# Optimization experiments

Hardware: AMD Instinct MI355X
Metric: run time of the kernel (lower is better)

Reference implementation:

```python
import jax, jax.numpy as jnp
import numpy as np

B, CIN, CMID, COUT, H, W = 4, 64, 128, 128, 128, 128
K = 9  # 3x3 taps
EPS = 1e-5


def conv3x3(x, w, b):
    # standard 3x3 conv, stride 1, pad 1, NCHW / OIHW
    y = jax.lax.conv_general_dilated(x, w, (1, 1), ((1, 1), (1, 1)),
                                     dimension_numbers=('NCHW', 'OIHW', 'NCHW'))
    return y + b[None, :, None, None]


def deform_conv3x3(x, offset, w, b):
    # torchvision DeformConv2d semantics (v1, no mask), kernel 3, pad 1, stride 1.
    # offset: [B, 2*K, H, W] with per-tap (dy, dx) pairs.
    Bn, C, Hn, Wn = x.shape
    off = offset.reshape(Bn, K, 2, Hn, Wn)
    off_y, off_x = off[:, :, 0], off[:, :, 1]          # [B,K,H,W]
    ky = (jnp.arange(K) // 3).astype(x.dtype)          # tap row 0..2
    kx = (jnp.arange(K) % 3).astype(x.dtype)           # tap col 0..2
    # sampling positions: p = out_pos - pad + tap + offset
    py = jnp.arange(Hn, dtype=x.dtype)[None, None, :, None] - 1.0 + ky[None, :, None, None] + off_y
    px = jnp.arange(Wn, dtype=x.dtype)[None, None, None, :] - 1.0 + kx[None, :, None, None] + off_x
    y0 = jnp.floor(py); x0 = jnp.floor(px)
    wy1 = py - y0; wx1 = px - x0                       # bilinear fractions
    y0i = y0.astype(jnp.int32); x0i = x0.astype(jnp.int32)
    xf = x.reshape(Bn, C, Hn * Wn)

    def gather(iy, ix):
        valid = ((iy >= 0) & (iy < Hn) & (ix >= 0) & (ix < Wn)).astype(x.dtype)
        idx = jnp.clip(iy, 0, Hn - 1) * Wn + jnp.clip(ix, 0, Wn - 1)  # [B,K,H,W]
        g = jax.vmap(lambda xb, ib: xb[:, ib])(xf, idx)               # [B,C,K,H,W]
        return g, valid

    g00, v00 = gather(y0i, x0i)
    g01, v01 = gather(y0i, x0i + 1)
    g10, v10 = gather(y0i + 1, x0i)
    g11, v11 = gather(y0i + 1, x0i + 1)

    def wmul(g, v, wgt):
        return g * (v * wgt)[:, None]                  # broadcast over channel dim

    sampled = (wmul(g00, v00, (1 - wy1) * (1 - wx1)) +
               wmul(g01, v01, (1 - wy1) * wx1) +
               wmul(g10, v10, wy1 * (1 - wx1)) +
               wmul(g11, v11, wy1 * wx1))              # [B,C,K,H,W]
    out = jnp.einsum('bckhw,ock->bohw', sampled, w.reshape(w.shape[0], C, K))
    return out + b[None, :, None, None]


def batchnorm_relu(x, gamma, beta):
    # training-mode BN: batch statistics over (N,H,W), biased variance
    mean = jnp.mean(x, axis=(0, 2, 3), keepdims=True)
    var = jnp.mean(jnp.square(x - mean), axis=(0, 2, 3), keepdims=True)
    y = (x - mean) * jax.lax.rsqrt(var + EPS)
    return jax.nn.relu(y * gamma[None, :, None, None] + beta[None, :, None, None])


def setup_inputs() -> dict:
    key = jax.random.key(0)
    ks = jax.random.split(key, 13)
    s = 0.05  # small weights keep offsets small / sampling mostly in-bounds
    return {
        'x': jax.random.normal(ks[0], (B, CIN, H, W), jnp.float32),
        'w_off1': jax.random.normal(ks[1], (2 * K, CIN, 3, 3), jnp.float32) * s,
        'b_off1': jnp.zeros((2 * K,), jnp.float32),
        'w1': jax.random.normal(ks[2], (CMID, CIN, 3, 3), jnp.float32) * s,
        'b1': jax.random.normal(ks[3], (CMID,), jnp.float32) * s,
        'g1': jnp.ones((CMID,), jnp.float32),
        'be1': jnp.zeros((CMID,), jnp.float32),
        'w_off2': jax.random.normal(ks[4], (2 * K, CMID, 3, 3), jnp.float32) * s,
        'b_off2': jnp.zeros((2 * K,), jnp.float32),
        'w2': jax.random.normal(ks[5], (COUT, CMID, 3, 3), jnp.float32) * s,
        'b2': jax.random.normal(ks[6], (COUT,), jnp.float32) * s,
        'g2': jnp.ones((COUT,), jnp.float32),
        'be2': jnp.zeros((COUT,), jnp.float32),
    }


def reference(x, w_off1, b_off1, w1, b1, g1, be1, w_off2, b_off2, w2, b2, g2, be2):
    offset1 = conv3x3(x, w_off1, b_off1)
    out = deform_conv3x3(x, offset1, w1, b1)
    out = batchnorm_relu(out, g1, be1)
    offset2 = conv3x3(out, w_off2, b_off2)
    out = deform_conv3x3(out, offset2, w2, b2)
    out = batchnorm_relu(out, g2, be2)
    return out
```

## Files before the change

kernel.cpp:

```cpp
#include <hip/hip_runtime.h>
#include <hip/hip_bf16.h>

#define BB 4
#define H_ 128
#define W_ 128
#define HWP 16384
#define CIN1 64
#define CMID 128
#define KOFF 18

typedef short short8 __attribute__((ext_vector_type(8)));
typedef float floatx4 __attribute__((ext_vector_type(4)));

#define WS_AB   16
#define WS_CVT  288
#define CVT_TOTAL 4447396
#define WS_WF1  4447744
#define WS_WF2  4484608
#define WS_XT   4558336
#define WS_OFF  6655488
#define WS_Y1   7835136
#define WS_Y1T  16223744
#define WS_WFO1 20418048
#define WS_WFO2 20436480
#define WS_PART 21600000
#define WS_Y2   WS_Y1

#define R_X     0
#define R_WOFF1 4194304
#define R_BOFF1 4204672
#define R_W1    4204690
#define R_B1    4278418
#define R_G1    4278546
#define R_BE1   4278674
#define R_WOFF2 4278802
#define R_BOFF2 4299538
#define R_W2    4299556
#define R_B2    4447012
#define R_G2    4447140
#define R_BE2   4447268

struct SrcPtrs { const void* p[13]; };

__device__ inline short f2bf(float f) {
    __hip_bfloat16 h = __float2bfloat16(f);
    return *reinterpret_cast<short*>(&h);
}
__device__ inline float bf2f(unsigned short u) {
    return __uint_as_float(((unsigned int)u) << 16);
}
__device__ inline float bfu_lo(unsigned int u) { return __uint_as_float(u << 16); }
__device__ inline float bfu_hi(unsigned int u) { return __uint_as_float(u & 0xFFFF0000u); }
__device__ inline float rl_f(float v, int i) {
    return __int_as_float(__builtin_amdgcn_readlane(__float_as_int(v), i));
}

__global__ void probe_dtype_k(const unsigned int* __restrict__ g1, int* __restrict__ flag) {
    if (threadIdx.x == 0 && blockIdx.x == 0) {
        flag[0] = ((g1[0] & 0xFFFFu) != 0u) ? 1 : 0;
    }
}

__global__ __launch_bounds__(256) void convert_inputs_k(SrcPtrs sp, float* __restrict__ dst,
                                                        const int* __restrict__ flag, int total) {
    int i = blockIdx.x * 256 + threadIdx.x;
    if (i >= total) return;
    constexpr int prefix[13] = {0, R_WOFF1, R_BOFF1, R_W1, R_B1, R_G1, R_BE1,
                                R_WOFF2, R_BOFF2, R_W2, R_B2, R_G2, R_BE2};
    const void* src = sp.p[0];
    int base = 0;
#pragma unroll
    for (int q = 1; q < 13; ++q) {
        if (i >= prefix[q]) { src = sp.p[q]; base = prefix[q]; }
    }
    int local = i - base;
    float v;
    if (flag[0] != 0) {
        v = bf2f(((const unsigned short*)src)[local]);
    } else {
        v = ((const float*)src)[local];
    }
    dst[i] = v;
}

template <int CIN>
__global__ __launch_bounds__(256) void wf_build_k(const float* __restrict__ w, short* __restrict__ wf) {
    constexpr int KSTEPS = CIN * 9 / 32;
    int idx = blockIdx.x * 256 + threadIdx.x;
    int j    = idx & 7;
    int lane = (idx >> 3) & 63;
    int rem  = idx >> 9;
    int ks   = rem % KSTEPS;
    int ct   = rem / KSTEPS;
    int co = ct * 16 + (lane & 15);
    int k  = ks * 32 + (lane >> 4) * 8 + j;
    int ci = k & (CIN - 1);
    int kk = k / CIN;
    wf[idx] = f2bf(w[(co * CIN + ci) * 9 + kk]);
}

template <int CIN>
__global__ __launch_bounds__(256) void wf_off_build_k(const float* __restrict__ w, short* __restrict__ wf) {
    constexpr int KSTEPS = CIN * 9 / 32;
    int idx = blockIdx.x * 256 + threadIdx.x;
    int j    = idx & 7;
    int lane = (idx >> 3) & 63;
    int rem  = idx >> 9;
    int ks   = rem % KSTEPS;
    int cc   = rem / KSTEPS;
    int sel  = cc >> 1;
    int co = (cc & 1) * 16 + (lane & 15);
    int k  = ks * 32 + (lane >> 4) * 8 + j;
    int ci = k & (CIN - 1);
    int kk = k / CIN;
    float v = (co < KOFF) ? w[(co * CIN + ci) * 9 + kk] : 0.f;
    short hi = f2bf(v);
    wf[idx] = sel ? f2bf(v - bf2f((unsigned short)hi)) : hi;
}

__global__ __launch_bounds__(256) void xt_build_k(const float* __restrict__ x,
                                                  unsigned short* __restrict__ xt,
                                                  unsigned short* __restrict__ xtl) {
    __shared__ __align__(4) short s_t[64 * 66];
    __shared__ __align__(4) short s_tl[64 * 66];
    int bi  = blockIdx.x;
    int hw0 = (bi & 255) * 64;
    int b   = bi >> 8;
    int t   = threadIdx.x;
    int hwp = t & 63;
#pragma unroll
    for (int it = 0; it < 16; ++it) {
        int c = it * 4 + (t >> 6);
        float v = x[((long)(b * 64 + c) << 14) + hw0 + hwp];
        short hi = f2bf(v);
        s_t[hwp * 66 + c]  = hi;
        s_tl[hwp * 66 + c] = f2bf(v - bf2f((unsigned short)hi));
    }
    __syncthreads();
#pragma unroll
    for (int it = 0; it < 8; ++it) {
        int i  = it * 256 + t;
        int c2 = (i & 31) * 2;
        int hw2 = i >> 5;
        long da = ((long)((b << 14) + hw0 + hw2)) * 64 + c2;
        *(int*)&xt[da]  = *(const int*)&s_t[hw2 * 66 + c2];
        *(int*)&xtl[da] = *(const int*)&s_tl[hw2 * 66 + c2];
    }
}

__device__ inline int conv_tpk(int h, int w0, int lane, int wv) {
    int tpk = 0;
    if (lane < 36) {
        int r = wv + 8 * lane;
        int p = r & 31;
        int k = r >> 5;
        int y = h - 1 + k / 3;
        int x = w0 + p - 1 + (k % 3);
        int valid = (y >= 0 && y < H_ && x >= 0 && x < W_) ? 1 : 0;
        int yc = min(max(y, 0), H_ - 1), xc = min(max(x, 0), W_ - 1);
        tpk = (yc * W_ + xc) | (valid << 16);
    }
    return tpk;
}

__device__ inline void convgather64(const unsigned short* __restrict__ xb, short* __restrict__ s_samp,
                                    int half, int li, int wv, int tpk) {
    constexpr int PADc = 584;
    unsigned int ub[18];
#pragma unroll
    for (int j = 0; j < 18; ++j) {
        int pkA = __builtin_amdgcn_readlane(tpk, 2 * j);
        int pkB = __builtin_amdgcn_readlane(tpk, 2 * j + 1);
        int pk = half ? pkB : pkA;
        unsigned int u = *(const unsigned int*)(xb + (pk & 0xFFFF) * 64 + 2 * li);
        ub[j] = (pk >> 16) ? u : 0u;
    }
#pragma unroll
    for (int j = 0; j < 18; ++j) {
        int r = wv + 8 * (half ? (2 * j + 1) : (2 * j));
        *(unsigned int*)&s_samp[(r & 31) * PADc + (r >> 5) * 64 + 2 * li] = ub[j];
    }
}

template <int I0, int NJ, int KKB>
__device__ inline void convgather128(const unsigned short* __restrict__ xb, short* __restrict__ s_samp,
                                     int lane, int wv, int tpk) {
    constexpr int PADc = 648;
    unsigned int ub[NJ];
#pragma unroll
    for (int j = 0; j < NJ; ++j) {
        int pk = __builtin_amdgcn_readlane(tpk, I0 + j);
        unsigned int u = *(const unsigned int*)(xb + (pk & 0xFFFF) * 128 + 2 * lane);
        ub[j] = (pk >> 16) ? u : 0u;
    }
#pragma unroll
    for (int j = 0; j < NJ; ++j) {
        int r = wv + 8 * (I0 + j);
        *(unsigned int*)&s_samp[(r & 31) * PADc + ((r >> 5) - KKB) * 128 + 2 * lane] = ub[j];
    }
}

__global__ __launch_bounds__(512, 4) void conv_off_mfma64_k(const unsigned short* __restrict__ xt,
                                                            const unsigned short* __restrict__ xtl,
                                                            const short* __restrict__ wfo,
                                                            const float* __restrict__ bias,
                                                            float* __restrict__ off) {
    constexpr int KSTEPS = 18;
    constexpr int PADc = 584;
    __shared__ __align__(16) short s_samp[32 * PADc];
    __shared__ float s_red[4 * 256];

    int bi = blockIdx.x;
    int w0 = (bi & 3) * 32;
    int h  = (bi >> 2) & 127;
    int b  = bi >> 9;
    int t  = threadIdx.x;
    int lane = t & 63;
    int wv   = t >> 6;

    int tpk = conv_tpk(h, w0, lane, wv);
    const unsigned short* xbh = xt  + (long)b * HWP * 64;
    const unsigned short* xbl = xtl + (long)b * HWP * 64;
    int half = lane >> 5, li = lane & 31;

    int p_   = lane & 15;
    int quad = lane >> 4;
    int c   = wv & 3;
    int ksl = wv >> 2;
    int ct  = c & 1;
    int pt  = c >> 1;
    int row = pt * 16 + p_;
    floatx4 acc;
#pragma unroll
    for (int r = 0; r < 4; ++r) {
        int co = ct * 16 + quad * 4 + r;
        acc[r] = (ksl == 0 && co < KOFF) ? bias[co] : 0.f;
    }

    convgather64(xbh, s_samp, half, li, wv, tpk);
    __syncthreads();
#pragma unroll
    for (int ki = 0; ki < 9; ++ki) {
        int ks = ksl * 9 + ki;
        short8 bfr = *(const short8*)&s_samp[row * PADc + ks * 32 + quad * 8];
        short8 ah  = *(const short8*)&wfo[(((long)ct * KSTEPS + ks) * 64 + lane) * 8];
        short8 al  = *(const short8*)&wfo[(((long)(2 + ct) * KSTEPS + ks) * 64 + lane) * 8];
        acc = __builtin_amdgcn_mfma_f32_16x16x32_bf16(ah, bfr, acc, 0, 0, 0);
        acc = __builtin_amdgcn_mfma_f32_16x16x32_bf16(al, bfr, acc, 0, 0, 0);
    }
    __syncthreads();

    convgather64(xbl, s_samp, half, li, wv, tpk);
    __syncthreads();
#pragma unroll
    for (int ki = 0; ki < 9; ++ki) {
        int ks = ksl * 9 + ki;
        short8 bfr = *(const short8*)&s_samp[row * PADc + ks * 32 + quad * 8];
        short8 ah  = *(const short8*)&wfo[(((long)ct * KSTEPS + ks) * 64 + lane) * 8];
        acc = __builtin_amdgcn_mfma_f32_16x16x32_bf16(ah, bfr, acc, 0, 0, 0);
    }

    if (ksl == 1) {
#pragma unroll
        for (int r = 0; r < 4; ++r) s_red[c * 256 + (quad * 4 + r) * 16 + p_] = acc[r];
    }
    __syncthreads();
    if (ksl == 0) {
#pragma unroll
        for (int r = 0; r < 4; ++r) {
            int co = ct * 16 + quad * 4 + r;
            if (co < KOFF) {
                float v = acc[r] + s_red[c * 256 + (quad * 4 + r) * 16 + p_];
                off[((long)(b * KOFF + co) << 14) + (h << 7) + w0 + pt * 16 + p_] = v;
            }
        }
    }
}

__global__ __launch_bounds__(512, 4) void conv_off_mfma128_k(const unsigned short* __restrict__ xt,
                                                             const unsigned short* __restrict__ xtl,
                                                             const short* __restrict__ wfo,
                                                             const float* __restrict__ bias,
                                                             float* __restrict__ off) {
    constexpr int KSTEPS = 36;
    constexpr int PADc = 648;
    __shared__ __align__(16) short s_samp[32 * PADc];
    __shared__ float s_red[4 * 256];

    int bi = blockIdx.x;
    int w0 = (bi & 3) * 32;
    int h  = (bi >> 2) & 127;
    int b  = bi >> 9;
    int t  = threadIdx.x;
    int lane = t & 63;
    int wv   = t >> 6;

    int tpk = conv_tpk(h, w0, lane, wv);
    const unsigned short* xbh = xt  + (long)b * HWP * 128;
    const unsigned short* xbl = xtl + (long)b * HWP * 128;

    int p_   = lane & 15;
    int quad = lane >> 4;
    int c   = wv & 3;
    int ksl = wv >> 2;
    int ct  = c & 1;
    int pt  = c >> 1;
    int row = pt * 16 + p_;
    floatx4 acc;
#pragma unroll
    for (int r = 0; r < 4; ++r) {
        int co = ct * 16 + quad * 4 + r;
        acc[r] = (ksl == 0 && co < KOFF) ? bias[co] : 0.f;
    }

    convgather128<0, 16, 0>(xbh, s_samp, lane, wv, tpk);
    __syncthreads();
#pragma unroll
    for (int ki = 0; ki < 8; ++ki) {
        int ks = ksl * 8 + ki;
        short8 bfr = *(const short8*)&s_samp[row * PADc + ks * 32 + quad * 8];
        short8 ah  = *(const short8*)&wfo[(((long)ct * KSTEPS + ks) * 64 + lane) * 8];
        short8 al  = *(const short8*)&wfo[(((long)(2 + ct) * KSTEPS + ks) * 64 + lane) * 8];
        acc = __builtin_amdgcn_mfma_f32_16x16x32_bf16(ah, bfr, acc, 0, 0, 0);
        acc = __builtin_amdgcn_mfma_f32_16x16x32_bf16(al, bfr, acc, 0, 0, 0);
    }
    __syncthreads();

    convgather128<16, 20, 4>(xbh, s_samp, lane, wv, tpk);
    __syncthreads();
#pragma unroll
    for (int ki = 0; ki < 10; ++ki) {
        int ks = 16 + ksl * 10 + ki;
        short8 bfr = *(const short8*)&s_samp[row * PADc + (ks - 16) * 32 + quad * 8];
        short8 ah  = *(const short8*)&wfo[(((long)ct * KSTEPS + ks) * 64 + lane) * 8];
        short8 al  = *(const short8*)&wfo[(((long)(2 + ct) * KSTEPS + ks) * 64 + lane) * 8];
        acc = __builtin_amdgcn_mfma_f32_16x16x32_bf16(ah, bfr, acc, 0, 0, 0);
        acc = __builtin_amdgcn_mfma_f32_16x16x32_bf16(al, bfr, acc, 0, 0, 0);
    }
    __syncthreads();

    convgather128<0, 16, 0>(xbl, s_samp, lane, wv, tpk);
    __syncthreads();
#pragma unroll
    for (int ki = 0; ki < 8; ++ki) {
        int ks = ksl * 8 + ki;
        short8 bfr = *(const short8*)&s_samp[row * PADc + ks * 32 + quad * 8];
        short8 ah  = *(const short8*)&wfo[(((long)ct * KSTEPS + ks) * 64 + lane) * 8];
        acc = __builtin_amdgcn_mfma_f32_16x16x32_bf16(ah, bfr, acc, 0, 0, 0);
    }
    __syncthreads();

    convgather128<16, 20, 4>(xbl, s_samp, lane, wv, tpk);
    __syncthreads();
#pragma unroll
    for (int ki = 0; ki < 10; ++ki) {
        int ks = 16 + ksl * 10 + ki;
        short8 bfr = *(const short8*)&s_samp[row * PADc + (ks - 16) * 32 + quad * 8];
        short8 ah  = *(const short8*)&wfo[(((long)ct * KSTEPS + ks) * 64 + lane) * 8];
        acc = __builtin_amdgcn_mfma_f32_16x16x32_bf16(ah, bfr, acc, 0, 0, 0);
    }

    if (ksl == 1) {
#pragma unroll
        for (int r = 0; r < 4; ++r) s_red[c * 256 + (quad * 4 + r) * 16 + p_] = acc[r];
    }
    __syncthreads();
    if (ksl == 0) {
#pragma unroll
        for (int r = 0; r < 4; ++r) {
            int co = ct * 16 + quad * 4 + r;
            if (co < KOFF) {
                float v = acc[r] + s_red[c * 256 + (quad * 4 + r) * 16 + p_];
                off[((long)(b * KOFF + co) << 14) + (h << 7) + w0 + pt * 16 + p_] = v;
            }
        }
    }
}

__device__ inline void build_table2(const float* __restrict__ off,
                                    int b, int h, int w0, int lane, int wv,
                                    int& tpk, float& tw0, float& tw1, float& tw2, float& tw3) {
    tpk = 0; tw0 = tw1 = tw2 = tw3 = 0.f;
    if (lane < 36) {
        int r = wv + 8 * lane;
        int p = r & 31;
        int k = r >> 5;
        int wpix = w0 + p;
        long obase = ((long)(b * KOFF) << 14) + (h << 7) + wpix;
        float oy = off[obase + ((long)(2 * k) << 14)];
        float ox = off[obase + ((long)(2 * k + 1) << 14)];
        float py = (float)(h - 1 + (k / 3)) + oy;
        float px = (float)(wpix - 1 + (k % 3)) + ox;
        float fy = floorf(py), fx = floorf(px);
        float wy = py - fy, wx = px - fx;
        int y0 = (int)fy, x0 = (int)fx;
        int y1 = y0 + 1, x1 = x0 + 1;
        bool vy0 = (y0 >= 0) && (y0 < H_);
        bool vy1 = (y1 >= 0) && (y1 < H_);
        bool vx0 = (x0 >= 0) && (x0 < W_);
        bool vx1 = (x1 >= 0) && (x1 < W_);
        float wy0 = 1.f - wy, wx0 = 1.f - wx;
        tw0 = (vy0 && vx0) ? wy0 * wx0 : 0.f;
        tw1 = (vy0 && vx1) ? wy0 * wx  : 0.f;
        tw2 = (vy1 && vx0) ? wy  * wx0 : 0.f;
        tw3 = (vy1 && vx1) ? wy  * wx  : 0.f;
        int iy0 = min(max(y0, 0), H_ - 1), iy1 = min(max(y1, 0), H_ - 1);
        int ix0 = min(max(x0, 0), W_ - 1), ix1 = min(max(x1, 0), W_ - 1);
        int dx = ix1 - ix0;
        int dy = iy1 - iy0;
        tpk = (iy0 * W_ + ix0) | (dx << 14) | (dy << 15);
    }
}

template <int NB>
__device__ inline void gather_batch128v2(const unsigned short* __restrict__ xb, short* __restrict__ s_samp,
                                         int i0, int kkbase, int wv, int lane,
                                         int tpk, float tw0, float tw1, float tw2, float tw3) {
    constexpr int PADc = 648;
    uint4 ub[NB];
#pragma unroll
    for (int j = 0; j < NB; ++j) {
        int pk = __builtin_amdgcn_readlane(tpk, i0 + j);
        const unsigned short* b00 = xb + (pk & 0x3FFF) * 128;
        const unsigned short* b01 = b00 + ((pk >> 14) & 1) * 128;
        const unsigned short* b10 = b00 + ((pk >> 15) & 1) * (W_ * 128);
        const unsigned short* b11 = b01 + ((pk >> 15) & 1) * (W_ * 128);
        ub[j].x = *(const unsigned int*)(b00 + 2 * lane);
        ub[j].y = *(const unsigned int*)(b01 + 2 * lane);
        ub[j].z = *(const unsigned int*)(b10 + 2 * lane);
        ub[j].w = *(const unsigned int*)(b11 + 2 * lane);
    }
#pragma unroll
    for (int j = 0; j < NB; ++j) {
        int i = i0 + j;
        int r = wv + 8 * i;
        float w00 = rl_f(tw0, i), w01 = rl_f(tw1, i), w10 = rl_f(tw2, i), w11 = rl_f(tw3, i);
        float vlo = w00 * bfu_lo(ub[j].x) + w01 * bfu_lo(ub[j].y)
                  + w10 * bfu_lo(ub[j].z) + w11 * bfu_lo(ub[j].w);
        float vhi = w00 * bfu_hi(ub[j].x) + w01 * bfu_hi(ub[j].y)
                  + w10 * bfu_hi(ub[j].z) + w11 * bfu_hi(ub[j].w);
        __hip_bfloat162 h2 = __float22bfloat162_rn(make_float2(vlo, vhi));
        *(unsigned int*)&s_samp[(r & 31) * PADc + ((r >> 5) - kkbase) * 128 + 2 * lane] =
            *reinterpret_cast<unsigned int*>(&h2);
    }
}

template <int NBP>
__device__ inline void gather_batch64v2(const unsigned short* __restrict__ xb, short* __restrict__ s_samp,
                                        int i0, int wv, int half, int li,
                                        int tpk, float tw0, float tw1, float tw2, float tw3) {
    constexpr int PADc = 584;
    uint4 ub[NBP];
#pragma unroll
    for (int j = 0; j < NBP; ++j) {
        int iA = i0 + 2 * j, iB = iA + 1;
        int pkA = __builtin_amdgcn_readlane(tpk, iA);
        int pkB = __builtin_amdgcn_readlane(tpk, iB);
        int pk = half ? pkB : pkA;
        const unsigned short* b00 = xb + (pk & 0x3FFF) * 64;
        const unsigned short* b01 = b00 + ((pk >> 14) & 1) * 64;
        const unsigned short* b10 = b00 + ((pk >> 15) & 1) * (W_ * 64);
        const unsigned short* b11 = b01 + ((pk >> 15) & 1) * (W_ * 64);
        ub[j].x = *(const unsigned int*)(b00 + 2 * li);
        ub[j].y = *(const unsigned int*)(b01 + 2 * li);
        ub[j].z = *(const unsigned int*)(b10 + 2 * li);
        ub[j].w = *(const unsigned int*)(b11 + 2 * li);
    }
#pragma unroll
    for (int j = 0; j < NBP; ++j) {
        int iA = i0 + 2 * j, iB = iA + 1;
        float w00 = half ? rl_f(tw0, iB) : rl_f(tw0, iA);
        float w01 = half ? rl_f(tw1, iB) : rl_f(tw1, iA);
        float w10 = half ? rl_f(tw2, iB) : rl_f(tw2, iA);
        float w11 = half ? rl_f(tw3, iB) : rl_f(tw3, iA);
        float vlo = w00 * bfu_lo(ub[j].x) + w01 * bfu_lo(ub[j].y)
                  + w10 * bfu_lo(ub[j].z) + w11 * bfu_lo(ub[j].w);
        float vhi = w00 * bfu_hi(ub[j].x) + w01 * bfu_hi(ub[j].y)
                  + w10 * bfu_hi(ub[j].z) + w11 * bfu_hi(ub[j].w);
        __hip_bfloat162 h2 = __float22bfloat162_rn(make_float2(vlo, vhi));
        int r = wv + 8 * (half ? iB : iA);
        *(unsigned int*)&s_samp[(r & 31) * PADc + (r >> 5) * 64 + 2 * li] =
            *reinterpret_cast<unsigned int*>(&h2);
    }
}

__global__ __launch_bounds__(512, 4) void deform_mfma64_k(const unsigned short* __restrict__ xt,
                                                          const float* __restrict__ off,
                                                          const short* __restrict__ wf,
                                                          const float* __restrict__ bias,
                                                          float* __restrict__ out) {
    constexpr int KSTEPS = 18;
    constexpr int PADc = 584;
    __shared__ __align__(16) short s_samp[32 * PADc];

    int bi = blockIdx.x;
    int w0 = (bi & 3) * 32;
    int h  = (bi >> 2) & 127;
    int b  = bi >> 9;
    int t  = threadIdx.x;
    int lane = t & 63;
    int wv   = t >> 6;

    int tpk; float tw0, tw1, tw2, tw3;
    build_table2(off, b, h, w0, lane, wv, tpk, tw0, tw1, tw2, tw3);
    const unsigned short* xb = xt + (long)b * HWP * 64;
    int half = lane >> 5, li = lane & 31;

    gather_batch64v2<6>(xb, s_samp,  0, wv, half, li, tpk, tw0, tw1, tw2, tw3);
    gather_batch64v2<6>(xb, s_samp, 12, wv, half, li, tpk, tw0, tw1, tw2, tw3);
    gather_batch64v2<6>(xb, s_samp, 24, wv, half, li, tpk, tw0, tw1, tw2, tw3);
    __syncthreads();

    int p_   = lane & 15;
    int quad = lane >> 4;
    int ct = wv;
    floatx4 acc0, acc1;
#pragma unroll
    for (int r = 0; r < 4; ++r) {
        float bv = bias[ct * 16 + quad * 4 + r];
        acc0[r] = bv;
        acc1[r] = bv;
    }
#pragma unroll 3
    for (int ks = 0; ks < KSTEPS; ++ks) {
        short8 a  = *(const short8*)&wf[(((long)ct * KSTEPS + ks) * 64 + lane) * 8];
        short8 b0 = *(const short8*)&s_samp[p_ * PADc + ks * 32 + quad * 8];
        short8 b1 = *(const short8*)&s_samp[(16 + p_) * PADc + ks * 32 + quad * 8];
        acc0 = __builtin_amdgcn_mfma_f32_16x16x32_bf16(a, b0, acc0, 0, 0, 0);
        acc1 = __builtin_amdgcn_mfma_f32_16x16x32_bf16(a, b1, acc1, 0, 0, 0);
    }

    long ob = ((long)(b * 128) << 14) + (h << 7) + w0 + p_;
#pragma unroll
    for (int r = 0; r < 4; ++r) {
        long cpl = (long)(ct * 16 + quad * 4 + r) << 14;
        out[ob + cpl]      = acc0[r];
        out[ob + 16 + cpl] = acc1[r];
    }
}

__global__ __launch_bounds__(512, 4) void deform_mfma128_k(const unsigned short* __restrict__ xt,
                                                           const float* __restrict__ off,
                                                           const short* __restrict__ wf,
                                                           const float* __restrict__ bias,
                                                           float* __restrict__ out) {
    constexpr int KSTEPS = 36;
    constexpr int PADc = 648;
    __shared__ __align__(16) short s_samp[32 * PADc];

    int bi = blockIdx.x;
    int w0 = (bi & 3) * 32;
    int h  = (bi >> 2) & 127;
    int b  = bi >> 9;
    int t  = threadIdx.x;
    int lane = t & 63;
    int wv   = t >> 6;

    int tpk; float tw0, tw1, tw2, tw3;
    build_table2(off, b, h, w0, lane, wv, tpk, tw0, tw1, tw2, tw3);
    const unsigned short* xb = xt + (long)b * HWP * 128;

    int p_   = lane & 15;
    int quad = lane >> 4;
    int ct = wv;
    floatx4 acc0, acc1;
#pragma unroll
    for (int r = 0; r < 4; ++r) {
        float bv = bias[ct * 16 + quad * 4 + r];
        acc0[r] = bv;
        acc1[r] = bv;
    }

    gather_batch128v2<8>(xb, s_samp, 0, 0, wv, lane, tpk, tw0, tw1, tw2, tw3);
    gather_batch128v2<8>(xb, s_samp, 8, 0, wv, lane, tpk, tw0, tw1, tw2, tw3);
    __syncthreads();
#pragma unroll 4
    for (int ks = 0; ks < 16; ++ks) {
        short8 a  = *(const short8*)&wf[(((long)ct * KSTEPS + ks) * 64 + lane) * 8];
        short8 b0 = *(const short8*)&s_samp[p_ * PADc + ks * 32 + quad * 8];
        short8 b1 = *(const short8*)&s_samp[(16 + p_) * PADc + ks * 32 + quad * 8];
        acc0 = __builtin_amdgcn_mfma_f32_16x16x32_bf16(a, b0, acc0, 0, 0, 0);
        acc1 = __builtin_amdgcn_mfma_f32_16x16x32_bf16(a, b1, acc1, 0, 0, 0);
    }
    __syncthreads();

    gather_batch128v2<5>(xb, s_samp, 16, 4, wv, lane, tpk, tw0, tw1, tw2, tw3);
    gather_batch128v2<5>(xb, s_samp, 21, 4, wv, lane, tpk, tw0, tw1, tw2, tw3);
    gather_batch128v2<5>(xb, s_samp, 26, 4, wv, lane, tpk, tw0, tw1, tw2, tw3);
    gather_batch128v2<5>(xb, s_samp, 31, 4, wv, lane, tpk, tw0, tw1, tw2, tw3);
    __syncthreads();
#pragma unroll 4
    for (int ks = 16; ks < KSTEPS; ++ks) {
        short8 a  = *(const short8*)&wf[(((long)ct * KSTEPS + ks) * 64 + lane) * 8];
        short8 b0 = *(const short8*)&s_samp[p_ * PADc + (ks - 16) * 32 + quad * 8];
        short8 b1 = *(const short8*)&s_samp[(16 + p_) * PADc + (ks - 16) * 32 + quad * 8];
        acc0 = __builtin_amdgcn_mfma_f32_16x16x32_bf16(a, b0, acc0, 0, 0, 0);
        acc1 = __builtin_amdgcn_mfma_f32_16x16x32_bf16(a, b1, acc1, 0, 0, 0);
    }

    long ob = ((long)(b * 128) << 14) + (h << 7) + w0 + p_;
#pragma unroll
    for (int r = 0; r < 4; ++r) {
        long cpl = (long)(ct * 16 + quad * 4 + r) << 14;
        out[ob + cpl]      = acc0[r];
        out[ob + 16 + cpl] = acc1[r];
    }
}

__global__ __launch_bounds__(256) void bn_stats_part_k(const float* __restrict__ y, float* __restrict__ part) {
    int bi = blockIdx.x;
    int c = bi & 127;
    int b = bi >> 7;
    int t = threadIdx.x;
    const float4* p4 = (const float4*)(y + ((long)(b * 128 + c) << 14));
    float sum = 0.f, ss = 0.f;
#pragma unroll
    for (int i = 0; i < 16; ++i) {
        float4 v = p4[t + 256 * i];
        sum += v.x + v.y + v.z + v.w;
        ss  += v.x * v.x + v.y * v.y + v.z * v.z + v.w * v.w;
    }
#pragma unroll
    for (int o = 32; o > 0; o >>= 1) { sum += __shfl_down(sum, o); ss += __shfl_down(ss, o); }
    __shared__ float s1[4], s2[4];
    int wave = t >> 6;
    if ((t & 63) == 0) { s1[wave] = sum; s2[wave] = ss; }
    __syncthreads();
    if (t == 0) {
        part[bi]       = s1[0] + s1[1] + s1[2] + s1[3];
        part[512 + bi] = s2[0] + s2[1] + s2[2] + s2[3];
    }
}

__global__ __launch_bounds__(256) void bn_apply_dual_k(float* __restrict__ y, const float* __restrict__ part,
                                                       const float* __restrict__ g, const float* __restrict__ be,
                                                       unsigned short* __restrict__ yt,
                                                       unsigned short* __restrict__ ytl) {
    __shared__ __align__(4) short s_t[64 * 134];
    __shared__ __align__(4) short s_tl[64 * 134];
    __shared__ float s_a[128], s_sh[128];
    int t = threadIdx.x;
    if (t < 128) {
        float sum = part[t] + part[128 + t] + part[256 + t] + part[384 + t];
        float ss  = part[512 + t] + part[640 + t] + part[768 + t] + part[896 + t];
        float mean = sum * (1.f / 65536.f);
        float var  = ss  * (1.f / 65536.f) - mean * mean;
        float inv  = rsqrtf(var + 1e-5f);
        float a = g[t] * inv;
        s_a[t]  = a;
        s_sh[t] = be[t] - mean * a;
    }
    __syncthreads();

    int bi  = blockIdx.x;
    int hw0 = (bi & 255) * 64;
    int b   = bi >> 8;
    int hwp = t & 63;
#pragma unroll 4
    for (int it = 0; it < 32; ++it) {
        int c = it * 4 + (t >> 6);
        float a = s_a[c], sh = s_sh[c];
        long addr = ((long)(b * 128 + c) << 14) + hw0 + hwp;
        float v = y[addr];
        v = fmaxf(v * a + sh, 0.f);
        y[addr] = v;
        short hi = f2bf(v);
        s_t[hwp * 134 + c]  = hi;
        s_tl[hwp * 134 + c] = f2bf(v - bf2f((unsigned short)hi));
    }
    __syncthreads();
#pragma unroll 4
    for (int it = 0; it < 16; ++it) {
        int i   = it * 256 + t;
        int c2  = (i & 63) * 2;
        int hw2 = i >> 6;
        long da = ((long)((b << 14) + hw0 + hw2)) * 128 + c2;
        *(int*)&yt[da]  = *(const int*)&s_t[hw2 * 134 + c2];
        *(int*)&ytl[da] = *(const int*)&s_tl[hw2 * 134 + c2];
    }
}

__global__ __launch_bounds__(256) void bn_apply_out_k(const float* __restrict__ y, const float* __restrict__ part,
                                                      const float* __restrict__ g, const float* __restrict__ be,
                                                      const int* __restrict__ flag, void* __restrict__ out, int total4) {
    __shared__ float s_a[128], s_sh[128];
    int t = threadIdx.x;
    if (t < 128) {
        float sum = part[t] + part[128 + t] + part[256 + t] + part[384 + t];
        float ss  = part[512 + t] + part[640 + t] + part[768 + t] + part[896 + t];
        float mean = sum * (1.f / 65536.f);
        float var  = ss  * (1.f / 65536.f) - mean * mean;
        float inv  = rsqrtf(var + 1e-5f);
        float a = g[t] * inv;
        s_a[t]  = a;
        s_sh[t] = be[t] - mean * a;
    }
    __syncthreads();

    int i = blockIdx.x * 256 + t;
    if (i >= total4) return;
    int c = (i >> 12) & 127;
    float a = s_a[c], sh = s_sh[c];
    float4 v = reinterpret_cast<const float4*>(y)[i];
    v.x = fmaxf(v.x * a + sh, 0.f);
    v.y = fmaxf(v.y * a + sh, 0.f);
    v.z = fmaxf(v.z * a + sh, 0.f);
    v.w = fmaxf(v.w * a + sh, 0.f);
    if (flag[0] != 0) {
        ushort4 u;
        u.x = (unsigned short)f2bf(v.x);
        u.y = (unsigned short)f2bf(v.y);
        u.z = (unsigned short)f2bf(v.z);
        u.w = (unsigned short)f2bf(v.w);
        reinterpret_cast<ushort4*>(out)[i] = u;
    } else {
        reinterpret_cast<float4*>(out)[i] = v;
    }
}

extern "C" void kernel_launch(void* const* d_in, const int* in_sizes, int n_in,
                              void* d_out, int out_size, void* d_ws, size_t ws_size,
                              hipStream_t stream) {
    float* ws   = (float*)d_ws;
    int*   flag = (int*)d_ws;
    float* cvt  = ws + WS_CVT;

    const float* X     = cvt + R_X;
    const float* Woff1 = cvt + R_WOFF1;
    const float* Boff1 = cvt + R_BOFF1;
    const float* W1f   = cvt + R_W1;
    const float* B1f   = cvt + R_B1;
    const float* G1    = cvt + R_G1;
    const float* Be1   = cvt + R_BE1;
    const float* Woff2 = cvt + R_WOFF2;
    const float* Boff2 = cvt + R_BOFF2;
    const float* W2f   = cvt + R_W2;
    const float* B2f   = cvt + R_B2;
    const float* G2    = cvt + R_G2;
    const float* Be2   = cvt + R_BE2;

    short* WF1  = (short*)(ws + WS_WF1);
    short* WF2  = (short*)(ws + WS_WF2);
    short* WFO1 = (short*)(ws + WS_WFO1);
    short* WFO2 = (short*)(ws + WS_WFO2);
    unsigned short* XT   = (unsigned short*)(ws + WS_XT);
    unsigned short* XTL  = (unsigned short*)(ws + WS_Y1);
    unsigned short* Y1T  = (unsigned short*)(ws + WS_Y1T);
    unsigned short* Y1TL = (unsigned short*)(ws + WS_CVT);
    float* OFF  = ws + WS_OFF;
    float* PART = ws + WS_PART;
    float* Y1   = ws + WS_Y1;
    float* Y2   = ws + WS_Y2;

    SrcPtrs sp;
    for (int j = 0; j < 13; ++j) sp.p[j] = d_in[j];

    probe_dtype_k<<<1, 64, 0, stream>>>((const unsigned int*)d_in[5], flag);
    convert_inputs_k<<<(CVT_TOTAL + 255) / 256, 256, 0, stream>>>(sp, cvt, flag, CVT_TOTAL);
    wf_build_k<64><<<288, 256, 0, stream>>>(W1f, WF1);
    wf_build_k<128><<<576, 256, 0, stream>>>(W2f, WF2);
    wf_off_build_k<64><<<144, 256, 0, stream>>>(Woff1, WFO1);
    wf_off_build_k<128><<<288, 256, 0, stream>>>(Woff2, WFO2);
    xt_build_k<<<1024, 256, 0, stream>>>(X, XT, XTL);

    conv_off_mfma64_k<<<BB * 128 * 4, 512, 0, stream>>>(XT, XTL, WFO1, Boff1, OFF);
    deform_mfma64_k<<<BB * 128 * 4, 512, 0, stream>>>(XT, OFF, WF1, B1f, Y1);
    bn_stats_part_k<<<512, 256, 0, stream>>>(Y1, PART);
    bn_apply_dual_k<<<1024, 256, 0, stream>>>(Y1, PART, G1, Be1, Y1T, Y1TL);

    conv_off_mfma128_k<<<BB * 128 * 4, 512, 0, stream>>>(Y1T, Y1TL, WFO2, Boff2, OFF);
    deform_mfma128_k<<<BB * 128 * 4, 512, 0, stream>>>(Y1T, OFF, WF2, B2f, Y2);
    bn_stats_part_k<<<512, 256, 0, stream>>>(Y2, PART);
    bn_apply_out_k<<<(BB * 128 * HWP / 4 + 255) / 256, 256, 0, stream>>>(Y2, PART, G2, Be2, flag, d_out, BB * 128 * HWP / 4);
}
```

Before: 343.2 us.

## Fuse offset conv into deformable conv kernels, keeping offsets in LDS

Merges the offset-predicting 3x3 conv kernel into the deformable conv kernel for both layers. Each block computes its 18 offset channels for the same 32-pixel tile, writes them to shared memory, and builds the bilinear sampling table from there. This removes two kernel launches and the global write and read of the offset tensor. XTL moves to its own workspace region because Y1 is now written while XTL is still being read. The cost is extra LDS (s_red, s_off) and register pressure, which may lower occupancy, and the offset conv and the deform work now run back to back inside each block.

New measurement: 330.8 us. 1.04x faster.

```diff
diff --git a/kernel.cpp b/kernel.cpp
--- a/kernel.cpp
+++ b/kernel.cpp
@@ -18,9 +18,9 @@
 #define WS_WF1  4447744
 #define WS_WF2  4484608
 #define WS_XT   4558336
-#define WS_OFF  6655488
 #define WS_Y1   7835136
 #define WS_Y1T  16223744
+#define WS_XTL  18320896
 #define WS_WFO1 20418048
 #define WS_WFO2 20436480
 #define WS_PART 21600000
@@ -200,195 +200,17 @@
     }
 }
 
-__global__ __launch_bounds__(512, 4) void conv_off_mfma64_k(const unsigned short* __restrict__ xt,
-                                                            const unsigned short* __restrict__ xtl,
-                                                            const short* __restrict__ wfo,
-                                                            const float* __restrict__ bias,
-                                                            float* __restrict__ off) {
-    constexpr int KSTEPS = 18;
-    constexpr int PADc = 584;
-    __shared__ __align__(16) short s_samp[32 * PADc];
-    __shared__ float s_red[4 * 256];
-
-    int bi = blockIdx.x;
-    int w0 = (bi & 3) * 32;
-    int h  = (bi >> 2) & 127;
-    int b  = bi >> 9;
-    int t  = threadIdx.x;
-    int lane = t & 63;
-    int wv   = t >> 6;
-
-    int tpk = conv_tpk(h, w0, lane, wv);
-    const unsigned short* xbh = xt  + (long)b * HWP * 64;
-    const unsigned short* xbl = xtl + (long)b * HWP * 64;
-    int half = lane >> 5, li = lane & 31;
-
-    int p_   = lane & 15;
-    int quad = lane >> 4;
-    int c   = wv & 3;
-    int ksl = wv >> 2;
-    int ct  = c & 1;
-    int pt  = c >> 1;
-    int row = pt * 16 + p_;
-    floatx4 acc;
-#pragma unroll
-    for (int r = 0; r < 4; ++r) {
-        int co = ct * 16 + quad * 4 + r;
-        acc[r] = (ksl == 0 && co < KOFF) ? bias[co] : 0.f;
-    }
-
-    convgather64(xbh, s_samp, half, li, wv, tpk);
-    __syncthreads();
-#pragma unroll
-    for (int ki = 0; ki < 9; ++ki) {
-        int ks = ksl * 9 + ki;
-        short8 bfr = *(const short8*)&s_samp[row * PADc + ks * 32 + quad * 8];
-        short8 ah  = *(const short8*)&wfo[(((long)ct * KSTEPS + ks) * 64 + lane) * 8];
-        short8 al  = *(const short8*)&wfo[(((long)(2 + ct) * KSTEPS + ks) * 64 + lane) * 8];
-        acc = __builtin_amdgcn_mfma_f32_16x16x32_bf16(ah, bfr, acc, 0, 0, 0);
-        acc = __builtin_amdgcn_mfma_f32_16x16x32_bf16(al, bfr, acc, 0, 0, 0);
-    }
-    __syncthreads();
-
-    convgather64(xbl, s_samp, half, li, wv, tpk);
-    __syncthreads();
-#pragma unroll
-    for (int ki = 0; ki < 9; ++ki) {
-        int ks = ksl * 9 + ki;
-        short8 bfr = *(const short8*)&s_samp[row * PADc + ks * 32 + quad * 8];
-        short8 ah  = *(const short8*)&wfo[(((long)ct * KSTEPS + ks) * 64 + lane) * 8];
-        acc = __builtin_amdgcn_mfma_f32_16x16x32_bf16(ah, bfr, acc, 0, 0, 0);
-    }
-
-    if (ksl == 1) {
-#pragma unroll
-        for (int r = 0; r < 4; ++r) s_red[c * 256 + (quad * 4 + r) * 16 + p_] = acc[r];
-    }
-    __syncthreads();
-    if (ksl == 0) {
-#pragma unroll
-        for (int r = 0; r < 4; ++r) {
-            int co = ct * 16 + quad * 4 + r;
-            if (co < KOFF) {
-                float v = acc[r] + s_red[c * 256 + (quad * 4 + r) * 16 + p_];
-                off[((long)(b * KOFF + co) << 14) + (h << 7) + w0 + pt * 16 + p_] = v;
-            }
-        }
-    }
-}
-
-__global__ __launch_bounds__(512, 4) void conv_off_mfma128_k(const unsigned short* __restrict__ xt,
-                                                             const unsigned short* __restrict__ xtl,
-                                                             const short* __restrict__ wfo,
-                                                             const float* __restrict__ bias,
-                                                             float* __restrict__ off) {
-    constexpr int KSTEPS = 36;
-    constexpr int PADc = 648;
-    __shared__ __align__(16) short s_samp[32 * PADc];
-    __shared__ float s_red[4 * 256];
-
-    int bi = blockIdx.x;
-    int w0 = (bi & 3) * 32;
-    int h  = (bi >> 2) & 127;
-    int b  = bi >> 9;
-    int t  = threadIdx.x;
-    int lane = t & 63;
-    int wv   = t >> 6;
-
-    int tpk = conv_tpk(h, w0, lane, wv);
-    const unsigned short* xbh = xt  + (long)b * HWP * 128;
-    const unsigned short* xbl = xtl + (long)b * HWP * 128;
-
-    int p_   = lane & 15;
-    int quad = lane >> 4;
-    int c   = wv & 3;
-    int ksl = wv >> 2;
-    int ct  = c & 1;
-    int pt  = c >> 1;
-    int row = pt * 16 + p_;
-    floatx4 acc;
-#pragma unroll
-    for (int r = 0; r < 4; ++r) {
-        int co = ct * 16 + quad * 4 + r;
-        acc[r] = (ksl == 0 && co < KOFF) ? bias[co] : 0.f;
-    }
-
-    convgather128<0, 16, 0>(xbh, s_samp, lane, wv, tpk);
-    __syncthreads();
-#pragma unroll
-    for (int ki = 0; ki < 8; ++ki) {
-        int ks = ksl * 8 + ki;
-        short8 bfr = *(const short8*)&s_samp[row * PADc + ks * 32 + quad * 8];
-        short8 ah  = *(const short8*)&wfo[(((long)ct * KSTEPS + ks) * 64 + lane) * 8];
-        short8 al  = *(const short8*)&wfo[(((long)(2 + ct) * KSTEPS + ks) * 64 + lane) * 8];
-        acc = __builtin_amdgcn_mfma_f32_16x16x32_bf16(ah, bfr, acc, 0, 0, 0);
-        acc = __builtin_amdgcn_mfma_f32_16x16x32_bf16(al, bfr, acc, 0, 0, 0);
-    }
-    __syncthreads();
-
-    convgather128<16, 20, 4>(xbh, s_samp, lane, wv, tpk);
-    __syncthreads();
-#pragma unroll
-    for (int ki = 0; ki < 10; ++ki) {
-        int ks = 16 + ksl * 10 + ki;
-        short8 bfr = *(const short8*)&s_samp[row * PADc + (ks - 16) * 32 + quad * 8];
-        short8 ah  = *(const short8*)&wfo[(((long)ct * KSTEPS + ks) * 64 + lane) * 8];
-        short8 al  = *(const short8*)&wfo[(((long)(2 + ct) * KSTEPS + ks) * 64 + lane) * 8];
-        acc = __builtin_amdgcn_mfma_f32_16x16x32_bf16(ah, bfr, acc, 0, 0, 0);
-        acc = __builtin_amdgcn_mfma_f32_16x16x32_bf16(al, bfr, acc, 0, 0, 0);
-    }
-    __syncthreads();
-
-    convgather128<0, 16, 0>(xbl, s_samp, lane, wv, tpk);
-    __syncthreads();
-#pragma unroll
-    for (int ki = 0; ki < 8; ++ki) {
-        int ks = ksl * 8 + ki;
-        short8 bfr = *(const short8*)&s_samp[row * PADc + ks * 32 + quad * 8];
-        short8 ah  = *(const short8*)&wfo[(((long)ct * KSTEPS + ks) * 64 + lane) * 8];
-        acc = __builtin_amdgcn_mfma_f32_16x16x32_bf16(ah, bfr, acc, 0, 0, 0);
-    }
-    __syncthreads();
-
-    convgather128<16, 20, 4>(xbl, s_samp, lane, wv, tpk);
-    __syncthreads();
-#pragma unroll
-    for (int ki = 0; ki < 10; ++ki) {
-        int ks = 16 + ksl * 10 + ki;
-        short8 bfr = *(const short8*)&s_samp[row * PADc + (ks - 16) * 32 + quad * 8];
-        short8 ah  = *(const short8*)&wfo[(((long)ct * KSTEPS + ks) * 64 + lane) * 8];
-        acc = __builtin_amdgcn_mfma_f32_16x16x32_bf16(ah, bfr, acc, 0, 0, 0);
-    }
-
-    if (ksl == 1) {
-#pragma unroll
-        for (int r = 0; r < 4; ++r) s_red[c * 256 + (quad * 4 + r) * 16 + p_] = acc[r];
-    }
-    __syncthreads();
-    if (ksl == 0) {
-#pragma unroll
-        for (int r = 0; r < 4; ++r) {
-            int co = ct * 16 + quad * 4 + r;
-            if (co < KOFF) {
-                float v = acc[r] + s_red[c * 256 + (quad * 4 + r) * 16 + p_];
-                off[((long)(b * KOFF + co) << 14) + (h << 7) + w0 + pt * 16 + p_] = v;
-            }
-        }
-    }
-}
-
-__device__ inline void build_table2(const float* __restrict__ off,
-                                    int b, int h, int w0, int lane, int wv,
-                                    int& tpk, float& tw0, float& tw1, float& tw2, float& tw3) {
+__device__ inline void build_table2_lds(const float* __restrict__ s_off,
+                                        int h, int w0, int lane, int wv,
+                                        int& tpk, float& tw0, float& tw1, float& tw2, float& tw3) {
     tpk = 0; tw0 = tw1 = tw2 = tw3 = 0.f;
     if (lane < 36) {
         int r = wv + 8 * lane;
         int p = r & 31;
         int k = r >> 5;
         int wpix = w0 + p;
-        long obase = ((long)(b * KOFF) << 14) + (h << 7) + wpix;
-        float oy = off[obase + ((long)(2 * k) << 14)];
-        float ox = off[obase + ((long)(2 * k + 1) << 14)];
+        float oy = s_off[(2 * k) * 32 + p];
+        float ox = s_off[(2 * k + 1) * 32 + p];
         float py = (float)(h - 1 + (k / 3)) + oy;
         float px = (float)(wpix - 1 + (k % 3)) + ox;
         float fy = floorf(py), fx = floorf(px);
@@ -484,14 +306,18 @@
     }
 }
 
-__global__ __launch_bounds__(512, 4) void deform_mfma64_k(const unsigned short* __restrict__ xt,
-                                                          const float* __restrict__ off,
-                                                          const short* __restrict__ wf,
-                                                          const float* __restrict__ bias,
-                                                          float* __restrict__ out) {
+__global__ __launch_bounds__(512, 4) void fused64_k(const unsigned short* __restrict__ xt,
+                                                    const unsigned short* __restrict__ xtl,
+                                                    const short* __restrict__ wfo,
+                                                    const float* __restrict__ boff,
+                                                    const short* __restrict__ wf,
+                                                    const float* __restrict__ bias,
+                                                    float* __restrict__ out) {
     constexpr int KSTEPS = 18;
     constexpr int PADc = 584;
     __shared__ __align__(16) short s_samp[32 * PADc];
+    __shared__ float s_red[4 * 256];
+    __shared__ float s_off[KOFF * 32];
 
     int bi = blockIdx.x;
     int w0 = (bi & 3) * 32;
@@ -501,18 +327,74 @@
     int lane = t & 63;
     int wv   = t >> 6;
 
-    int tpk; float tw0, tw1, tw2, tw3;
-    build_table2(off, b, h, w0, lane, wv, tpk, tw0, tw1, tw2, tw3);
-    const unsigned short* xb = xt + (long)b * HWP * 64;
+    const unsigned short* xbh = xt  + (long)b * HWP * 64;
+    const unsigned short* xbl = xtl + (long)b * HWP * 64;
     int half = lane >> 5, li = lane & 31;
-
-    gather_batch64v2<6>(xb, s_samp,  0, wv, half, li, tpk, tw0, tw1, tw2, tw3);
-    gather_batch64v2<6>(xb, s_samp, 12, wv, half, li, tpk, tw0, tw1, tw2, tw3);
-    gather_batch64v2<6>(xb, s_samp, 24, wv, half, li, tpk, tw0, tw1, tw2, tw3);
-    __syncthreads();
-
     int p_   = lane & 15;
     int quad = lane >> 4;
+
+    {
+        int tpkc = conv_tpk(h, w0, lane, wv);
+        int c   = wv & 3;
+        int ksl = wv >> 2;
+        int ct  = c & 1;
+        int pt  = c >> 1;
+        int row = pt * 16 + p_;
+        floatx4 acc;
+#pragma unroll
+        for (int r = 0; r < 4; ++r) {
+            int co = ct * 16 + quad * 4 + r;
+            acc[r] = (ksl == 0 && co < KOFF) ? boff[co] : 0.f;
+        }
+
+        convgather64(xbh, s_samp, half, li, wv, tpkc);
+        __syncthreads();
+#pragma unroll
+        for (int ki = 0; ki < 9; ++ki) {
+            int ks = ksl * 9 + ki;
+            short8 bfr = *(const short8*)&s_samp[row * PADc + ks * 32 + quad * 8];
+            short8 ah  = *(const short8*)&wfo[(((long)ct * KSTEPS + ks) * 64 + lane) * 8];
+            short8 al  = *(const short8*)&wfo[(((long)(2 + ct) * KSTEPS + ks) * 64 + lane) * 8];
+            acc = __builtin_amdgcn_mfma_f32_16x16x32_bf16(ah, bfr, acc, 0, 0, 0);
+            acc = __builtin_amdgcn_mfma_f32_16x16x32_bf16(al, bfr, acc, 0, 0, 0);
+        }
+        __syncthreads();
+
+        convgather64(xbl, s_samp, half, li, wv, tpkc);
+        __syncthreads();
+#pragma unroll
+        for (int ki = 0; ki < 9; ++ki) {
+            int ks = ksl * 9 + ki;
+            short8 bfr = *(const short8*)&s_samp[row * PADc + ks * 32 + quad * 8];
+            short8 ah  = *(const short8*)&wfo[(((long)ct * KSTEPS + ks) * 64 + lane) * 8];
+            acc = __builtin_amdgcn_mfma_f32_16x16x32_bf16(ah, bfr, acc, 0, 0, 0);
+        }
+
+        if (ksl == 1) {
+#pragma unroll
+            for (int r = 0; r < 4; ++r) s_red[c * 256 + (quad * 4 + r) * 16 + p_] = acc[r];
+        }
+        __syncthreads();
+        if (ksl == 0) {
+#pragma unroll
+            for (int r = 0; r < 4; ++r) {
+                int co = ct * 16 + quad * 4 + r;
+                if (co < KOFF) {
+                    s_off[co * 32 + pt * 16 + p_] = acc[r] + s_red[c * 256 + (quad * 4 + r) * 16 + p_];
+                }
+            }
+        }
+        __syncthreads();
+    }
+
+    int tpk; float tw0, tw1, tw2, tw3;
+    build_table2_lds(s_off, h, w0, lane, wv, tpk, tw0, tw1, tw2, tw3);
+
+    gather_batch64v2<6>(xbh, s_samp,  0, wv, half, li, tpk, tw0, tw1, tw2, tw3);
+    gather_batch64v2<6>(xbh, s_samp, 12, wv, half, li, tpk, tw0, tw1, tw2, tw3);
+    gather_batch64v2<6>(xbh, s_samp, 24, wv, half, li, tpk, tw0, tw1, tw2, tw3);
+    __syncthreads();
+
     int ct = wv;
     floatx4 acc0, acc1;
 #pragma unroll
@@ -539,14 +421,18 @@
     }
 }
 
-__global__ __launch_bounds__(512, 4) void deform_mfma128_k(const unsigned short* __restrict__ xt,
-                                                           const float* __restrict__ off,
-                                                           const short* __restrict__ wf,
-                                                           const float* __restrict__ bias,
-                                                           float* __restrict__ out) {
+__global__ __launch_bounds__(512, 4) void fused128_k(const unsigned short* __restrict__ xt,
+                                                     const unsigned short* __restrict__ xtl,
+                                                     const short* __restrict__ wfo,
+                                                     const float* __restrict__ boff,
+                                                     const short* __restrict__ wf,
+                                                     const float* __restrict__ bias,
+                                                     float* __restrict__ out) {
     constexpr int KSTEPS = 36;
     constexpr int PADc = 648;
     __shared__ __align__(16) short s_samp[32 * PADc];
+    __shared__ float s_red[4 * 256];
+    __shared__ float s_off[KOFF * 32];
 
     int bi = blockIdx.x;
     int w0 = (bi & 3) * 32;
@@ -556,12 +442,92 @@
     int lane = t & 63;
     int wv   = t >> 6;
 
-    int tpk; float tw0, tw1, tw2, tw3;
-    build_table2(off, b, h, w0, lane, wv, tpk, tw0, tw1, tw2, tw3);
-    const unsigned short* xb = xt + (long)b * HWP * 128;
-
+    const unsigned short* xbh = xt  + (long)b * HWP * 128;
+    const unsigned short* xbl = xtl + (long)b * HWP * 128;
     int p_   = lane & 15;
     int quad = lane >> 4;
+
+    {
+        int tpkc = conv_tpk(h, w0, lane, wv);
+        int c   = wv & 3;
+        int ksl = wv >> 2;
+        int ct  = c & 1;
+        int pt  = c >> 1;
+        int row = pt * 16 + p_;
+        floatx4 acc;
+#pragma unroll
+        for (int r = 0; r < 4; ++r) {
+            int co = ct * 16 + quad * 4 + r;
+            acc[r] = (ksl == 0 && co < KOFF) ? boff[co] : 0.f;
+        }
+
+        convgather128<0, 16, 0>(xbh, s_samp, lane, wv, tpkc);
+        __syncthreads();
+#pragma unroll
+        for (int ki = 0; ki < 8; ++ki) {
+            int ks = ksl * 8 + ki;
+            short8 bfr = *(const short8*)&s_samp[row * PADc + ks * 32 + quad * 8];
+            short8 ah  = *(const short8*)&wfo[(((long)ct * KSTEPS + ks) * 64 + lane) * 8];
+            short8 al  = *(const short8*)&wfo[(((long)(2 + ct) * KSTEPS + ks) * 64 + lane) * 8];
+            acc = __builtin_amdgcn_mfma_f32_16x16x32_bf16(ah, bfr, acc, 0, 0, 0);
+            acc = __builtin_amdgcn_mfma_f32_16x16x32_bf16(al, bfr, acc, 0, 0, 0);
+        }
+        __syncthreads();
+
+        convgather128<16, 20, 4>(xbh, s_samp, lane, wv, tpkc);
+        __syncthreads();
+#pragma unroll
+        for (int ki = 0; ki < 10; ++ki) {
+            int ks = 16 + ksl * 10 + ki;
+            short8 bfr = *(const short8*)&s_samp[row * PADc + (ks - 16) * 32 + quad * 8];
+            short8 ah  = *(const short8*)&wfo[(((long)ct * KSTEPS + ks) * 64 + lane) * 8];
+            short8 al  = *(const short8*)&wfo[(((long)(2 + ct) * KSTEPS + ks) * 64 + lane) * 8];
+            acc = __builtin_amdgcn_mfma_f32_16x16x32_bf16(ah, bfr, acc, 0, 0, 0);
+            acc = __builtin_amdgcn_mfma_f32_16x16x32_bf16(al, bfr, acc, 0, 0, 0);
+        }
+        __syncthreads();
+
+        convgather128<0, 16, 0>(xbl, s_samp, lane, wv, tpkc);
+        __syncthreads();
+#pragma unroll
+        for (int ki = 0; ki < 8; ++ki) {
+            int ks = ksl * 8 + ki;
+            short8 bfr = *(const short8*)&s_samp[row * PADc + ks * 32 + quad * 8];
+            short8 ah  = *(const short8*)&wfo[(((long)ct * KSTEPS + ks) * 64 + lane) * 8];
+            acc = __builtin_amdgcn_mfma_f32_16x16x32_bf16(ah, bfr, acc, 0, 0, 0);
+        }
+        __syncthreads();
+
+        convgather128<16, 20, 4>(xbl, s_samp, lane, wv, tpkc);
+        __syncthreads();
+#pragma unroll
+        for (int ki = 0; ki < 10; ++ki) {
+            int ks = 16 + ksl * 10 + ki;
+            short8 bfr = *(const short8*)&s_samp[row * PADc + (ks - 16) * 32 + quad * 8];
+            short8 ah  = *(const short8*)&wfo[(((long)ct * KSTEPS + ks) * 64 + lane) * 8];
+            acc = __builtin_amdgcn_mfma_f32_16x16x32_bf16(ah, bfr, acc, 0, 0, 0);
+        }
+
+        if (ksl == 1) {
+#pragma unroll
+            for (int r = 0; r < 4; ++r) s_red[c * 256 + (quad * 4 + r) * 16 + p_] = acc[r];
+        }
+        __syncthreads();
+        if (ksl == 0) {
+#pragma unroll
+            for (int r = 0; r < 4; ++r) {
+                int co = ct * 16 + quad * 4 + r;
+                if (co < KOFF) {
+                    s_off[co * 32 + pt * 16 + p_] = acc[r] + s_red[c * 256 + (quad * 4 + r) * 16 + p_];
+                }
+            }
+        }
+        __syncthreads();
+    }
+
+    int tpk; float tw0, tw1, tw2, tw3;
+    build_table2_lds(s_off, h, w0, lane, wv, tpk, tw0, tw1, tw2, tw3);
+
     int ct = wv;
     floatx4 acc0, acc1;
 #pragma unroll
@@ -571,8 +537,8 @@
         acc1[r] = bv;
     }
 
-    gather_batch128v2<8>(xb, s_samp, 0, 0, wv, lane, tpk, tw0, tw1, tw2, tw3);
-    gather_batch128v2<8>(xb, s_samp, 8, 0, wv, lane, tpk, tw0, tw1, tw2, tw3);
+    gather_batch128v2<8>(xbh, s_samp, 0, 0, wv, lane, tpk, tw0, tw1, tw2, tw3);
+    gather_batch128v2<8>(xbh, s_samp, 8, 0, wv, lane, tpk, tw0, tw1, tw2, tw3);
     __syncthreads();
 #pragma unroll 4
     for (int ks = 0; ks < 16; ++ks) {
@@ -584,10 +550,10 @@
     }
     __syncthreads();
 
-    gather_batch128v2<5>(xb, s_samp, 16, 4, wv, lane, tpk, tw0, tw1, tw2, tw3);
-    gather_batch128v2<5>(xb, s_samp, 21, 4, wv, lane, tpk, tw0, tw1, tw2, tw3);
-    gather_batch128v2<5>(xb, s_samp, 26, 4, wv, lane, tpk, tw0, tw1, tw2, tw3);
-    gather_batch128v2<5>(xb, s_samp, 31, 4, wv, lane, tpk, tw0, tw1, tw2, tw3);
+    gather_batch128v2<5>(xbh, s_samp, 16, 4, wv, lane, tpk, tw0, tw1, tw2, tw3);
+    gather_batch128v2<5>(xbh, s_samp, 21, 4, wv, lane, tpk, tw0, tw1, tw2, tw3);
+    gather_batch128v2<5>(xbh, s_samp, 26, 4, wv, lane, tpk, tw0, tw1, tw2, tw3);
+    gather_batch128v2<5>(xbh, s_samp, 31, 4, wv, lane, tpk, tw0, tw1, tw2, tw3);
     __syncthreads();
 #pragma unroll 4
     for (int ks = 16; ks < KSTEPS; ++ks) {
@@ -744,10 +710,9 @@
     short* WFO1 = (short*)(ws + WS_WFO1);
     short* WFO2 = (short*)(ws + WS_WFO2);
     unsigned short* XT   = (unsigned short*)(ws + WS_XT);
-    unsigned short* XTL  = (unsigned short*)(ws + WS_Y1);
+    unsigned short* XTL  = (unsigned short*)(ws + WS_XTL);
     unsigned short* Y1T  = (unsigned short*)(ws + WS_Y1T);
     unsigned short* Y1TL = (unsigned short*)(ws + WS_CVT);
-    float* OFF  = ws + WS_OFF;
     float* PART = ws + WS_PART;
     float* Y1   = ws + WS_Y1;
     float* Y2   = ws + WS_Y2;
@@ -763,13 +728,11 @@
     wf_off_build_k<128><<<288, 256, 0, stream>>>(Woff2, WFO2);
     xt_build_k<<<1024, 256, 0, stream>>>(X, XT, XTL);
 
-    conv_off_mfma64_k<<<BB * 128 * 4, 512, 0, stream>>>(XT, XTL, WFO1, Boff1, OFF);
-    deform_mfma64_k<<<BB * 128 * 4, 512, 0, stream>>>(XT, OFF, WF1, B1f, Y1);
+    fused64_k<<<BB * 128 * 4, 512, 0, stream>>>(XT, XTL, WFO1, Boff1, WF1, B1f, Y1);
     bn_stats_part_k<<<512, 256, 0, stream>>>(Y1, PART);
     bn_apply_dual_k<<<1024, 256, 0, stream>>>(Y1, PART, G1, Be1, Y1T, Y1TL);
 
-    conv_off_mfma128_k<<<BB * 128 * 4, 512, 0, stream>>>(Y1T, Y1TL, WFO2, Boff2, OFF);
-    deform_mfma128_k<<<BB * 128 * 4, 512, 0, stream>>>(Y1T, OFF, WF2, B2f, Y2);
+    fused128_k<<<BB * 128 * 4, 512, 0, stream>>>(Y1T, Y1TL, WFO2, Boff2, WF2, B2f, Y2);
     bn_stats_part_k<<<512, 256, 0, stream>>>(Y2, PART);
     bn_apply_out_k<<<(BB * 128 * HWP / 4 + 255) / 256, 256, 0, stream>>>(Y2, PART, G2, Be2, flag, d_out, BB * 128 * HWP / 4);
 }
```
